# Kernel optimization log

Hardware: AMD Instinct MI355X
Metric: run time of the kernel (lower is better)

## Reference

```python
import jax, jax.numpy as jnp
import numpy as np

B, L, C, E, H = 16, 1024, 4, 256, 8
DH = E // H
LN_EPS = 1e-5

def setup_inputs() -> dict:
    key = jax.random.key(0)
    ks = jax.random.split(key, 7)
    return {
        "input_seq": jax.random.randint(ks[0], (B, L), 0, C),
        "emb_w": jax.random.normal(ks[1], (L, E, C), dtype=jnp.float32) * 0.05,
        "emb_b": jax.random.normal(ks[2], (L, E), dtype=jnp.float32) * 0.05,
        "in_proj_w": jax.random.normal(ks[3], (3 * E, E), dtype=jnp.float32) * 0.05,
        "in_proj_b": jax.random.normal(ks[4], (3 * E,), dtype=jnp.float32) * 0.05,
        "out_w": jax.random.normal(ks[5], (E, E), dtype=jnp.float32) * 0.05,
        "out_b": jax.random.normal(ks[6], (E,), dtype=jnp.float32) * 0.05,
    }

def _layer_norm(x):
    m = jnp.mean(x, axis=-1, keepdims=True)
    v = jnp.var(x, axis=-1, keepdims=True)
    return (x - m) / jnp.sqrt(v + LN_EPS)

def reference(input_seq, emb_w, emb_b, in_proj_w, in_proj_b, out_w, out_b):
    # one-hot @ per-site weight == direct gather: emb[b,l,:] = emb_w[l,:,input_seq[b,l]]
    wt = jnp.transpose(emb_w, (0, 2, 1))          # [L, C, E]
    l_idx = jnp.arange(L)[None, :]                # [1, L]
    embedded = wt[l_idx, input_seq] + emb_b       # [B, L, E]
    embedded = _layer_norm(embedded)

    # nn.MultiheadAttention(batch_first=True), self-attention
    qkv = embedded @ in_proj_w.T + in_proj_b      # [B, L, 3E]
    q, k, v = jnp.split(qkv, 3, axis=-1)
    q = q.reshape(B, L, H, DH)
    k = k.reshape(B, L, H, DH)
    v = v.reshape(B, L, H, DH)
    scores = jnp.einsum("blhd,bmhd->bhlm", q, k) / jnp.sqrt(jnp.float32(DH))
    attn = jax.nn.softmax(scores, axis=-1)
    ctx = jnp.einsum("bhlm,bmhd->blhd", attn, v).reshape(B, L, E)
    attn_out = ctx @ out_w.T + out_b              # [B, L, E]

    return _layer_norm(attn_out + embedded)
```

## Files before the change

kernel.cpp:

```cpp
#include <hip/hip_runtime.h>

#define B_  16
#define L_  1024
#define E_  256
#define H_  8
#define DH_ 32
#define M_  (B_ * L_)
#define SCALE_L2E 0.25501817656f

typedef unsigned short u16;
typedef unsigned int   u32;
typedef short bf8_t __attribute__((ext_vector_type(8)));
typedef float f4_t  __attribute__((ext_vector_type(4)));
typedef float f16f  __attribute__((ext_vector_type(16)));
union F4U { uint4 u; bf8_t s; };

static __device__ __forceinline__ float bf2f(u16 u) {
    return __uint_as_float(((u32)u) << 16);
}
static __device__ __forceinline__ u16 f2bf(float f) {
    u32 u = __float_as_uint(f);
    u32 r = 0x7FFFu + ((u >> 16) & 1u);
    return (u16)((u + r) >> 16);
}
static __device__ __forceinline__ u32 cvt_pk_bf16(float a, float b) {
    u32 r;
    asm("v_cvt_pk_bf16_f32 %0, %1, %2" : "=v"(r) : "v"(a), "v"(b));
    return r;
}
static __device__ __forceinline__ void pswap(u32 &a, u32 &b) {
    asm("v_permlane32_swap_b32 %0, %1" : "+v"(a), "+v"(b));
}

__global__ __launch_bounds__(256) void table_conv_k(
    const float* __restrict__ emb_w,
    const float* __restrict__ emb_b,
    const float* __restrict__ in_proj_w,
    const float* __restrict__ out_w,
    u16* __restrict__ tbl,
    u16* __restrict__ wcvt)
{
    int blk = blockIdx.x, tid = threadIdx.x;
    {
        int idx = blk * 256 + tid;
        float v = (idx < 196608) ? in_proj_w[idx] : out_w[idx - 196608];
        wcvt[idx] = f2bf(v);
    }
    int w = tid >> 6, lane = tid & 63;
    int l = blk, c = w;
    const float* wp = emb_w + (size_t)l * 1024 + c;
    float4 bb = *(const float4*)(emb_b + (size_t)l * 256 + lane * 4);
    float bv[4] = {bb.x, bb.y, bb.z, bb.w};
    float x[4], s = 0.f, q = 0.f;
    #pragma unroll
    for (int j = 0; j < 4; ++j) {
        float t = wp[(lane * 4 + j) * 4] + bv[j];
        x[j] = t; s += t; q += t * t;
    }
    #pragma unroll
    for (int off = 1; off < 64; off <<= 1) {
        s += __shfl_xor(s, off);
        q += __shfl_xor(q, off);
    }
    float mean = s * (1.0f / 256.0f);
    float var  = q * (1.0f / 256.0f) - mean * mean;
    float rstd = rsqrtf(var + 1e-5f);
    ushort4 o = { f2bf((x[0] - mean) * rstd), f2bf((x[1] - mean) * rstd),
                  f2bf((x[2] - mean) * rstd), f2bf((x[3] - mean) * rstd) };
    *(ushort4*)(tbl + ((size_t)l * 4 + c) * 256 + lane * 4) = o;
}

__global__ __launch_bounds__(256) void gemm_qkv_mfma_k(
    const int* __restrict__ seq,
    const u16* __restrict__ tbl,
    const u16* __restrict__ wqkv,
    const float* __restrict__ bias,
    u16* __restrict__ q_s, u16* __restrict__ k_s, u16* __restrict__ vt)
{
    int tid = threadIdx.x;
    int w = tid >> 6, lane = tid & 63, l15 = lane & 15, quad = lane >> 4;
    int n0 = blockIdx.x * 64, m0 = blockIdx.y * 256;
    int b = m0 >> 10;

    const u16* Apt[4];
    #pragma unroll
    for (int t = 0; t < 4; ++t) {
        int m = m0 + w * 64 + t * 16 + l15;
        int cls = seq[m];
        Apt[t] = tbl + ((size_t)((m & 1023) * 4 + cls)) * 256 + quad * 8;
    }
    const u16* Bp = wqkv + (size_t)(n0 + l15) * 256 + quad * 8;

    f4_t acc[4][4] = {{{0,0,0,0},{0,0,0,0},{0,0,0,0},{0,0,0,0}},
                      {{0,0,0,0},{0,0,0,0},{0,0,0,0},{0,0,0,0}},
                      {{0,0,0,0},{0,0,0,0},{0,0,0,0},{0,0,0,0}},
                      {{0,0,0,0},{0,0,0,0},{0,0,0,0},{0,0,0,0}}};

    if (n0 < 512) {
        #pragma unroll
        for (int ks = 0; ks < 8; ++ks) {
            F4U bfr[4];
            #pragma unroll
            for (int nc = 0; nc < 4; ++nc)
                bfr[nc].u = *(const uint4*)(Bp + nc * 16 * 256 + ks * 32);
            #pragma unroll
            for (int t = 0; t < 4; ++t) {
                F4U a; a.u = *(const uint4*)(Apt[t] + ks * 32);
                #pragma unroll
                for (int nc = 0; nc < 4; ++nc)
                    acc[t][nc] = __builtin_amdgcn_mfma_f32_16x16x32_bf16(bfr[nc].s, a.s, acc[t][nc], 0, 0, 0);
            }
        }
        float sc = (n0 < 256) ? SCALE_L2E : 1.0f;
        u16* dst = (n0 < 256) ? q_s : k_s;
        #pragma unroll
        for (int t = 0; t < 4; ++t) {
            int l = (m0 & 1023) + w * 64 + t * 16 + l15;
            #pragma unroll
            for (int nc = 0; nc < 4; ++nc) {
                int nb = n0 + nc * 16 + quad * 4;
                float4 b4 = *(const float4*)(bias + nb);
                int nl = nb & 255, h = nl >> 5, d0 = nl & 31;
                ushort4 o = { f2bf((acc[t][nc][0] + b4.x) * sc), f2bf((acc[t][nc][1] + b4.y) * sc),
                              f2bf((acc[t][nc][2] + b4.z) * sc), f2bf((acc[t][nc][3] + b4.w) * sc) };
                *(ushort4*)(dst + ((size_t)(b * 8 + h) * 1024 + l) * 32 + d0) = o;
            }
        }
    } else {
        #pragma unroll
        for (int ks = 0; ks < 8; ++ks) {
            F4U bfr[4];
            #pragma unroll
            for (int nc = 0; nc < 4; ++nc)
                bfr[nc].u = *(const uint4*)(Bp + nc * 16 * 256 + ks * 32);
            #pragma unroll
            for (int t = 0; t < 4; ++t) {
                F4U a; a.u = *(const uint4*)(Apt[t] + ks * 32);
                #pragma unroll
                for (int nc = 0; nc < 4; ++nc)
                    acc[t][nc] = __builtin_amdgcn_mfma_f32_16x16x32_bf16(a.s, bfr[nc].s, acc[t][nc], 0, 0, 0);
            }
        }
        #pragma unroll
        for (int t = 0; t < 4; ++t) {
            int lq = (m0 & 1023) + w * 64 + t * 16 + quad * 4;
            #pragma unroll
            for (int nc = 0; nc < 4; ++nc) {
                int n = n0 + nc * 16 + l15;
                float bv = bias[n];
                int nl = n & 255, h = nl >> 5, d = nl & 31;
                ushort4 o = { f2bf(acc[t][nc][0] + bv), f2bf(acc[t][nc][1] + bv),
                              f2bf(acc[t][nc][2] + bv), f2bf(acc[t][nc][3] + bv) };
                *(ushort4*)(vt + ((size_t)(b * 8 + h) * 32 + d) * 1024 + lq) = o;
            }
        }
    }
}

__global__ __launch_bounds__(256, 2) void attn32_k(
    const u16* __restrict__ q_s,
    const u16* __restrict__ k_s,
    const u16* __restrict__ vt,
    u16* __restrict__ ctx)
{
    int tid = threadIdx.x;
    int w = tid >> 6, lane = tid & 63, col = lane & 31, hi = lane >> 5;
    int g = blockIdx.x;
    int bh = (g & 7) | ((g >> 5) << 3);
    int q0 = ((g >> 3) & 3) * 256 + w * 64;

    const u16* kb = k_s + ((((size_t)bh << 10) + col) << 5) + hi * 8;
    const u16* vb = vt + ((((size_t)bh << 5) + col) << 10) + hi * 8;

    F4U qf[2][2];
    #pragma unroll
    for (int t = 0; t < 2; ++t)
        #pragma unroll
        for (int s = 0; s < 2; ++s)
            qf[t][s].u = *(const uint4*)(q_s + ((((size_t)bh << 10) + q0 + t * 32 + col) << 5) + s * 16 + hi * 8);

    f16f Z;
    #pragma unroll
    for (int r = 0; r < 16; ++r) Z[r] = 0.f;

    f16f O[2];
    #pragma unroll
    for (int t = 0; t < 2; ++t)
        #pragma unroll
        for (int r = 0; r < 16; ++r) O[t][r] = 0.f;
    float psum[2] = {0.f, 0.f};

    F4U kA[2][2], kB[2][2], vA[2][2], vB[2][2];
    auto LD = [&](F4U (&kf)[2][2], F4U (&vf)[2][2], int key0) {
        #pragma unroll
        for (int h = 0; h < 2; ++h)
            #pragma unroll
            for (int s = 0; s < 2; ++s) {
                kf[h][s].u = *(const uint4*)(kb + (size_t)(key0 + h * 32) * 32 + s * 16);
                vf[h][s].u = *(const uint4*)(vb + key0 + h * 32 + s * 16);
            }
    };
    auto STEP = [&](F4U (&kf)[2][2], F4U (&vf)[2][2]) {
        f16f S[2][2];
        __builtin_amdgcn_s_setprio(1);
        #pragma unroll
        for (int t = 0; t < 2; ++t)
            #pragma unroll
            for (int h = 0; h < 2; ++h) {
                S[t][h] = __builtin_amdgcn_mfma_f32_32x32x16_bf16(kf[h][0].s, qf[t][0].s, Z, 0, 0, 0);
                S[t][h] = __builtin_amdgcn_mfma_f32_32x32x16_bf16(kf[h][1].s, qf[t][1].s, S[t][h], 0, 0, 0);
            }
        __builtin_amdgcn_s_setprio(0);
        F4U pf[2][2][2];
        #pragma unroll
        for (int t = 0; t < 2; ++t)
            #pragma unroll
            for (int h = 0; h < 2; ++h) {
                float p[16];
                #pragma unroll
                for (int r = 0; r < 16; ++r) p[r] = __builtin_amdgcn_exp2f(S[t][h][r]);
                psum[t] += ((((p[0] + p[1]) + (p[2] + p[3])) + ((p[4] + p[5]) + (p[6] + p[7])))
                          + (((p[8] + p[9]) + (p[10] + p[11])) + ((p[12] + p[13]) + (p[14] + p[15]))));
                u32 W0 = cvt_pk_bf16(p[0],  p[1]),  W1 = cvt_pk_bf16(p[2],  p[3]);
                u32 W2 = cvt_pk_bf16(p[4],  p[5]),  W3 = cvt_pk_bf16(p[6],  p[7]);
                u32 W4 = cvt_pk_bf16(p[8],  p[9]),  W5 = cvt_pk_bf16(p[10], p[11]);
                u32 W6 = cvt_pk_bf16(p[12], p[13]), W7 = cvt_pk_bf16(p[14], p[15]);
                pswap(W0, W2); pswap(W1, W3);
                pswap(W4, W6); pswap(W5, W7);
                pf[t][h][0].u = make_uint4(W0, W1, W2, W3);
                pf[t][h][1].u = make_uint4(W4, W5, W6, W7);
            }
        __builtin_amdgcn_s_setprio(1);
        #pragma unroll
        for (int t = 0; t < 2; ++t) {
            O[t] = __builtin_amdgcn_mfma_f32_32x32x16_bf16(vf[0][0].s, pf[t][0][0].s, O[t], 0, 0, 0);
            O[t] = __builtin_amdgcn_mfma_f32_32x32x16_bf16(vf[0][1].s, pf[t][0][1].s, O[t], 0, 0, 0);
            O[t] = __builtin_amdgcn_mfma_f32_32x32x16_bf16(vf[1][0].s, pf[t][1][0].s, O[t], 0, 0, 0);
            O[t] = __builtin_amdgcn_mfma_f32_32x32x16_bf16(vf[1][1].s, pf[t][1][1].s, O[t], 0, 0, 0);
        }
        __builtin_amdgcn_s_setprio(0);
    };

    LD(kA, vA, 0);
    for (int u = 0; u < 16; u += 2) {
        LD(kB, vB, (u + 1) * 64);
        STEP(kA, vA);
        if (u + 2 < 16) LD(kA, vA, (u + 2) * 64);
        STEP(kB, vB);
    }

    #pragma unroll
    for (int t = 0; t < 2; ++t) {
        float ps = psum[t];
        ps += __shfl_xor(ps, 32);
        float inv = 1.0f / ps;
        u16* op = ctx + ((((size_t)bh << 10) + q0 + t * 32 + col) << 5) + hi * 4;
        #pragma unroll
        for (int gi = 0; gi < 4; ++gi) {
            uint2 st;
            st.x = cvt_pk_bf16(O[t][4 * gi + 0] * inv, O[t][4 * gi + 1] * inv);
            st.y = cvt_pk_bf16(O[t][4 * gi + 2] * inv, O[t][4 * gi + 3] * inv);
            *(uint2*)(op + gi * 8) = st;
        }
    }
}

__global__ __launch_bounds__(256) void proj_ln_k(
    const int* __restrict__ seq,
    const u16* __restrict__ ctx,
    const u16* __restrict__ wout,
    const float* __restrict__ out_b,
    const u16* __restrict__ tbl,
    float* __restrict__ out)
{
    __shared__ float2 sm[4][16];
    int tid = threadIdx.x;
    int w = tid >> 6, lane = tid & 63, l15 = lane & 15, quad = lane >> 4;
    int m0 = blockIdx.x * 16;
    int b = m0 >> 10, lbase = (m0 & 1023) + l15;

    const u16* Bp = wout + (size_t)(w * 64 + l15) * 256 + quad * 8;

    f4_t acc[4] = {{0,0,0,0},{0,0,0,0},{0,0,0,0},{0,0,0,0}};

    #pragma unroll
    for (int ks = 0; ks < 8; ++ks) {
        F4U a; a.u = *(const uint4*)(ctx + ((size_t)(b * 8 + ks) * 1024 + lbase) * 32 + quad * 8);
        #pragma unroll
        for (int nc = 0; nc < 4; ++nc) {
            F4U bf; bf.u = *(const uint4*)(Bp + (size_t)nc * 16 * 256 + ks * 32);
            acc[nc] = __builtin_amdgcn_mfma_f32_16x16x32_bf16(bf.s, a.s, acc[nc], 0, 0, 0);
        }
    }

    int row = m0 + l15;
    int cls = seq[row];
    const u16* ep = tbl + ((size_t)((row & 1023) * 4 + cls)) * 256;
    float s = 0.f, q = 0.f;
    #pragma unroll
    for (int nc = 0; nc < 4; ++nc) {
        int nb = w * 64 + nc * 16 + quad * 4;
        float4 bb = *(const float4*)(out_b + nb);
        ushort4 e4 = *(const ushort4*)(ep + nb);
        acc[nc][0] += bb.x + bf2f(e4.x);
        acc[nc][1] += bb.y + bf2f(e4.y);
        acc[nc][2] += bb.z + bf2f(e4.z);
        acc[nc][3] += bb.w + bf2f(e4.w);
        #pragma unroll
        for (int r = 0; r < 4; ++r) { s += acc[nc][r]; q += acc[nc][r] * acc[nc][r]; }
    }
    s += __shfl_xor(s, 16);  q += __shfl_xor(q, 16);
    s += __shfl_xor(s, 32);  q += __shfl_xor(q, 32);
    if (quad == 0) sm[w][l15] = make_float2(s, q);
    __syncthreads();
    float2 t0 = sm[0][l15], t1 = sm[1][l15], t2 = sm[2][l15], t3 = sm[3][l15];
    s = (t0.x + t1.x) + (t2.x + t3.x);
    q = (t0.y + t1.y) + (t2.y + t3.y);
    float mean = s * (1.0f / 256.0f);
    float var  = q * (1.0f / 256.0f) - mean * mean;
    float rstd = rsqrtf(var + 1e-5f);
    #pragma unroll
    for (int nc = 0; nc < 4; ++nc) {
        float4 o = { (acc[nc][0] - mean) * rstd, (acc[nc][1] - mean) * rstd,
                     (acc[nc][2] - mean) * rstd, (acc[nc][3] - mean) * rstd };
        *(float4*)(out + (size_t)row * 256 + w * 64 + nc * 16 + quad * 4) = o;
    }
}

extern "C" void kernel_launch(void* const* d_in, const int* in_sizes, int n_in,
                              void* d_out, int out_size, void* d_ws, size_t ws_size,
                              hipStream_t stream) {
    const int*   seq       = (const int*)d_in[0];
    const float* emb_w     = (const float*)d_in[1];
    const float* emb_b     = (const float*)d_in[2];
    const float* in_proj_w = (const float*)d_in[3];
    const float* in_proj_b = (const float*)d_in[4];
    const float* out_w     = (const float*)d_in[5];
    const float* out_b     = (const float*)d_in[6];
    float*       out       = (float*)d_out;

    const size_t P   = (size_t)M_ * 256;
    const size_t TBL = (size_t)L_ * 4 * 256;
    u16* ws   = (u16*)d_ws;
    u16* tbl  = ws;
    u16* q_s  = ws + TBL;
    u16* k_s  = q_s + P;
    u16* vt   = k_s + P;
    u16* ctx  = vt + P;
    u16* wqkv = ctx + P;
    u16* wout = wqkv + 768 * 256;

    table_conv_k<<<1024, 256, 0, stream>>>(emb_w, emb_b, in_proj_w, out_w, tbl, wqkv);
    gemm_qkv_mfma_k<<<dim3(12, 64), 256, 0, stream>>>(seq, tbl, wqkv, in_proj_b, q_s, k_s, vt);
    attn32_k<<<512, 256, 0, stream>>>(q_s, k_s, vt, ctx);
    proj_ln_k<<<M_ / 16, 256, 0, stream>>>(seq, ctx, wout, out_b, tbl, out);
}
```

Before: 167.6 us.

## Software-pipeline attention so exp of one key tile overlaps next QK MFMAs

The attention inner loop is restructured so that QK^T MFMAs for the next key tile are interleaved with the exp2/pack work on the current tile's scores. K and V loads are split so K for tile u+2 is issued early and V is reloaded right after its PV use. The goal is to hide transcendental and VALU latency behind matrix-core work instead of running them in series. The cost is one wasted QK computation and extra wrapped loads at the end of the loop, plus higher register pressure from keeping S, pf and four K/V buffers live.

```diff
diff --git a/kernel.cpp b/kernel.cpp
--- a/kernel.cpp
+++ b/kernel.cpp
@@ -190,46 +190,44 @@
         for (int r = 0; r < 16; ++r) O[t][r] = 0.f;
     float psum[2] = {0.f, 0.f};
 
-    F4U kA[2][2], kB[2][2], vA[2][2], vB[2][2];
-    auto LD = [&](F4U (&kf)[2][2], F4U (&vf)[2][2], int key0) {
+    f16f S[2][2];
+    F4U  pf[2][2][2];
+    F4U  k0[2][2], k1[2][2], v0[2][2], v1[2][2];
+
+    auto LDK = [&](F4U (&kf)[2][2], int key0) {
         #pragma unroll
         for (int h = 0; h < 2; ++h)
             #pragma unroll
-            for (int s = 0; s < 2; ++s) {
+            for (int s = 0; s < 2; ++s)
                 kf[h][s].u = *(const uint4*)(kb + (size_t)(key0 + h * 32) * 32 + s * 16);
+    };
+    auto LDV = [&](F4U (&vf)[2][2], int key0) {
+        #pragma unroll
+        for (int h = 0; h < 2; ++h)
+            #pragma unroll
+            for (int s = 0; s < 2; ++s)
                 vf[h][s].u = *(const uint4*)(vb + key0 + h * 32 + s * 16);
-            }
-    };
-    auto STEP = [&](F4U (&kf)[2][2], F4U (&vf)[2][2]) {
-        f16f S[2][2];
-        __builtin_amdgcn_s_setprio(1);
-        #pragma unroll
-        for (int t = 0; t < 2; ++t)
-            #pragma unroll
-            for (int h = 0; h < 2; ++h) {
-                S[t][h] = __builtin_amdgcn_mfma_f32_32x32x16_bf16(kf[h][0].s, qf[t][0].s, Z, 0, 0, 0);
-                S[t][h] = __builtin_amdgcn_mfma_f32_32x32x16_bf16(kf[h][1].s, qf[t][1].s, S[t][h], 0, 0, 0);
-            }
-        __builtin_amdgcn_s_setprio(0);
-        F4U pf[2][2][2];
-        #pragma unroll
-        for (int t = 0; t < 2; ++t)
-            #pragma unroll
-            for (int h = 0; h < 2; ++h) {
-                float p[16];
-                #pragma unroll
-                for (int r = 0; r < 16; ++r) p[r] = __builtin_amdgcn_exp2f(S[t][h][r]);
-                psum[t] += ((((p[0] + p[1]) + (p[2] + p[3])) + ((p[4] + p[5]) + (p[6] + p[7])))
-                          + (((p[8] + p[9]) + (p[10] + p[11])) + ((p[12] + p[13]) + (p[14] + p[15]))));
-                u32 W0 = cvt_pk_bf16(p[0],  p[1]),  W1 = cvt_pk_bf16(p[2],  p[3]);
-                u32 W2 = cvt_pk_bf16(p[4],  p[5]),  W3 = cvt_pk_bf16(p[6],  p[7]);
-                u32 W4 = cvt_pk_bf16(p[8],  p[9]),  W5 = cvt_pk_bf16(p[10], p[11]);
-                u32 W6 = cvt_pk_bf16(p[12], p[13]), W7 = cvt_pk_bf16(p[14], p[15]);
-                pswap(W0, W2); pswap(W1, W3);
-                pswap(W4, W6); pswap(W5, W7);
-                pf[t][h][0].u = make_uint4(W0, W1, W2, W3);
-                pf[t][h][1].u = make_uint4(W4, W5, W6, W7);
-            }
+    };
+    auto QKC = [&](F4U (&kf)[2][2], int t, int h) {
+        S[t][h] = __builtin_amdgcn_mfma_f32_32x32x16_bf16(kf[h][0].s, qf[t][0].s, Z, 0, 0, 0);
+        S[t][h] = __builtin_amdgcn_mfma_f32_32x32x16_bf16(kf[h][1].s, qf[t][1].s, S[t][h], 0, 0, 0);
+    };
+    auto EXPPACK = [&](int t, int h) {
+        float p[16];
+        #pragma unroll
+        for (int r = 0; r < 16; ++r) p[r] = __builtin_amdgcn_exp2f(S[t][h][r]);
+        psum[t] += ((((p[0] + p[1]) + (p[2] + p[3])) + ((p[4] + p[5]) + (p[6] + p[7])))
+                  + (((p[8] + p[9]) + (p[10] + p[11])) + ((p[12] + p[13]) + (p[14] + p[15]))));
+        u32 W0 = cvt_pk_bf16(p[0],  p[1]),  W1 = cvt_pk_bf16(p[2],  p[3]);
+        u32 W2 = cvt_pk_bf16(p[4],  p[5]),  W3 = cvt_pk_bf16(p[6],  p[7]);
+        u32 W4 = cvt_pk_bf16(p[8],  p[9]),  W5 = cvt_pk_bf16(p[10], p[11]);
+        u32 W6 = cvt_pk_bf16(p[12], p[13]), W7 = cvt_pk_bf16(p[14], p[15]);
+        pswap(W0, W2); pswap(W1, W3);
+        pswap(W4, W6); pswap(W5, W7);
+        pf[t][h][0].u = make_uint4(W0, W1, W2, W3);
+        pf[t][h][1].u = make_uint4(W4, W5, W6, W7);
+    };
+    auto PV = [&](F4U (&vf)[2][2]) {
         __builtin_amdgcn_s_setprio(1);
         #pragma unroll
         for (int t = 0; t < 2; ++t) {
@@ -241,12 +239,28 @@
         __builtin_amdgcn_s_setprio(0);
     };
 
-    LD(kA, vA, 0);
-    for (int u = 0; u < 16; u += 2) {
-        LD(kB, vB, (u + 1) * 64);
-        STEP(kA, vA);
-        if (u + 2 < 16) LD(kA, vA, (u + 2) * 64);
-        STEP(kB, vB);
+    LDK(k0, 0);   LDV(v0, 0);
+    LDK(k1, 64);  LDV(v1, 64);
+    QKC(k0, 0, 0); QKC(k0, 0, 1); QKC(k0, 1, 0); QKC(k0, 1, 1);
+
+    for (int i = 0; i < 8; ++i) {
+        int u  = 2 * i;
+        int a2 = ((u + 2) & 15) * 64;
+        int a3 = ((u + 3) & 15) * 64;
+        LDK(k0, a2);
+        EXPPACK(0, 0); QKC(k1, 0, 0);
+        EXPPACK(0, 1); QKC(k1, 0, 1);
+        EXPPACK(1, 0); QKC(k1, 1, 0);
+        EXPPACK(1, 1); QKC(k1, 1, 1);
+        PV(v0);
+        LDV(v0, a2);
+        LDK(k1, a3);
+        EXPPACK(0, 0); QKC(k0, 0, 0);
+        EXPPACK(0, 1); QKC(k0, 0, 1);
+        EXPPACK(1, 0); QKC(k0, 1, 0);
+        EXPPACK(1, 1); QKC(k0, 1, 1);
+        PV(v1);
+        LDV(v1, a3);
     }
 
     #pragma unroll
```

New measurement: 172.4 us. 1.03x slower.
